# Optimization experiments

Measured on AMD Instinct MI355X. Metric: run time of the kernel, lower is better.

## Reference

```python
import jax, jax.numpy as jnp
import numpy as np

B, CIN, COUT, K, H, W = 8, 256, 256, 3, 128, 128


def setup_inputs() -> dict:
    key = jax.random.key(0)
    k1, k2, k3 = jax.random.split(key, 3)
    return {
        "input_vector": jax.random.normal(k1, (B, CIN, H, W), dtype=jnp.float32),
        "style_vector": jax.random.normal(k2, (B, CIN), dtype=jnp.float32),
        "weight": jax.random.normal(k3, (COUT, CIN, K, K), dtype=jnp.float32),
    }


def reference(input_vector, style_vector, weight):
    b, cin, h, w = input_vector.shape
    cout, _, k, _ = weight.shape
    # per-sample modulated weights: (b, O, I, k, k)
    ws = weight[None, :, :, :, :] * style_vector[:, None, :, None, None]
    # NOTE: faithful to source - sum over dims [1,2,3] = (O, I, kh), NOT kw.
    demod = jax.lax.rsqrt(jnp.sum(ws * ws, axis=(1, 2, 3), keepdims=True) + 1e-8)  # (b,1,1,1,k)
    ws = (ws * demod).reshape(b * cout, cin, k, k)
    x = input_vector.reshape(1, b * cin, h, w)
    # get_same_padding(W, k, dilation=1, stride=1) = (k-1)//2
    pad = ((w - 1) * (1 - 1) + 1 * (k - 1)) // 2
    out = jax.lax.conv_general_dilated(
        x, ws,
        window_strides=(1, 1),
        padding=[(pad, pad), (pad, pad)],
        feature_group_count=b,
        dimension_numbers=("NCHW", "OIHW", "NCHW"),
    )
    out = out.reshape(b, cout, h, w)
    return jax.nn.leaky_relu(out, negative_slope=0.2)
```

## Files before the change

kernel.cpp:

```cpp
#include <hip/hip_runtime.h>
#include <hip/hip_bf16.h>

#define B_    8
#define CIN   256
#define COUT  256
#define H_    128
#define W_    128
#define HP    130
#define WP    130

#define OCT   128
#define TROWS 8
#define TCOLS 32
#define XROWS 10
#define XCOLS 34
#define XCH   1360
#define XCHP  1536
#define CCS   ((size_t)COUT * CIN)

using bfrag = __attribute__((ext_vector_type(8))) short;
using f32x4 = __attribute__((ext_vector_type(4))) float;

#define ASM_VMCNT(n) asm volatile("s_waitcnt vmcnt(" #n ")" ::: "memory")
#define ASM_LGKM0()  asm volatile("s_waitcnt lgkmcnt(0)" ::: "memory")

__device__ __forceinline__ float leaky(float v) {
    return v >= 0.f ? v : 0.2f * v;
}

__device__ __forceinline__ unsigned short to_bf16(float v) {
    __hip_bfloat16 h = __float2bfloat16(v);
    return *(unsigned short*)&h;
}

__global__ void compute_S_kernel(const float* __restrict__ weight, float* __restrict__ S) {
    const int i = blockIdx.x;
    const int t = threadIdx.x;
    const float* wp = weight + ((size_t)t * CIN + i) * 9;
    float s0 = 0.f, s1 = 0.f, s2 = 0.f;
#pragma unroll
    for (int kh = 0; kh < 3; ++kh) {
        float a = wp[kh * 3 + 0], b = wp[kh * 3 + 1], c = wp[kh * 3 + 2];
        s0 = fmaf(a, a, s0); s1 = fmaf(b, b, s1); s2 = fmaf(c, c, s2);
    }
    __shared__ float red[3][256];
    red[0][t] = s0; red[1][t] = s1; red[2][t] = s2;
    __syncthreads();
    for (int off = 128; off > 0; off >>= 1) {
        if (t < off) {
            red[0][t] += red[0][t + off];
            red[1][t] += red[1][t + off];
            red[2][t] += red[2][t + off];
        }
        __syncthreads();
    }
    if (t == 0) {
        S[i * 3 + 0] = red[0][0];
        S[i * 3 + 1] = red[1][0];
        S[i * 3 + 2] = red[2][0];
    }
}

__global__ void compute_demod_kernel(const float* __restrict__ style,
                                     const float* __restrict__ S,
                                     float* __restrict__ demod) {
    const int b = blockIdx.x;
    const int t = threadIdx.x;
    float sv = style[b * CIN + t];
    float sv2 = sv * sv;
    float s0 = sv2 * S[t * 3 + 0];
    float s1 = sv2 * S[t * 3 + 1];
    float s2 = sv2 * S[t * 3 + 2];
    __shared__ float red[3][256];
    red[0][t] = s0; red[1][t] = s1; red[2][t] = s2;
    __syncthreads();
    for (int off = 128; off > 0; off >>= 1) {
        if (t < off) {
            red[0][t] += red[0][t + off];
            red[1][t] += red[1][t + off];
            red[2][t] += red[2][t + off];
        }
        __syncthreads();
    }
    if (t == 0) {
        demod[b * 3 + 0] = rsqrtf(red[0][0] + 1e-8f);
        demod[b * 3 + 1] = rsqrtf(red[1][0] + 1e-8f);
        demod[b * 3 + 2] = rsqrtf(red[2][0] + 1e-8f);
    }
}

__global__ void compute_wmodT_kernel(const float* __restrict__ weight,
                                     const float* __restrict__ style,
                                     const float* __restrict__ demod,
                                     unsigned short* __restrict__ wT) {
    const int bx = blockIdx.x;
    const int i  = threadIdx.x;
    const int o  = bx & (COUT - 1);
    const int j  = (bx >> 8) % 9;
    const int b  = bx / (9 * COUT);
    float w = weight[((size_t)o * CIN + i) * 9 + j];
    float m = style[b * CIN + i] * demod[b * 3 + (j % 3)];
    wT[(((size_t)(b * 9 + j) * COUT + o)) * CIN + i] = to_bf16(w * m);
}

__global__ __launch_bounds__(256) void transpose_kernel(const float* __restrict__ x,
                                                        unsigned short* __restrict__ xT) {
    const int bx = blockIdx.x;
    const int wtile = (bx & 3) * 32;
    const int itile = (bx >> 2) * 32;
    const int h = blockIdx.y;
    const int b = blockIdx.z;
    const int t = threadIdx.x;

    __shared__ float lt[32][33];

    {
        const int tw = t & 31, tr = t >> 5;
#pragma unroll
        for (int rr = 0; rr < 4; ++rr) {
            int il = tr + rr * 8;
            lt[il][tw] = x[(((size_t)b * CIN + itile + il) * H_ + h) * W_ + wtile + tw];
        }
    }
    __syncthreads();
    {
        const int il = t & 31, wr = t >> 5;
#pragma unroll
        for (int rr = 0; rr < 4; ++rr) {
            int wl = wr + rr * 8;
            xT[(((size_t)b * HP + (h + 1)) * WP + (wtile + wl + 1)) * CIN + itile + il] =
                to_bf16(lt[il][wl]);
        }
    }
}

__global__ void zero_border_kernel(unsigned short* __restrict__ xT) {
    const int b = blockIdx.x;
    const int r = blockIdx.y;
    const int t = threadIdx.x;
    int npix, base, stride;
    if (r == 0)      { npix = WP;  base = 0;                 stride = 1;  }
    else if (r == 1) { npix = WP;  base = (HP - 1) * WP;     stride = 1;  }
    else if (r == 2) { npix = 128; base = WP;                stride = WP; }
    else             { npix = 128; base = WP + (WP - 1);     stride = WP; }
    for (int idx = t; idx < npix * 32; idx += 256) {
        int p = idx >> 5, q = idx & 31;
        size_t off = ((size_t)b * HP * WP + base + (size_t)p * stride) * CIN;
        *(int4*)((unsigned short*)xT + off + q * 8) = (int4){0, 0, 0, 0};
    }
}

__global__ __launch_bounds__(256, 2) void conv_mfma_kernel(
    const unsigned short* __restrict__ xT,
    const unsigned short* __restrict__ wT,
    float* __restrict__ out)
{
    const int tid = threadIdx.x;
    const int lin = blockIdx.x;
    const int b    = lin & 7;
    const int rest = lin >> 3;
    const int oc0  = (rest & 1) * OCT;
    const int w0   = ((rest >> 1) & 3) * TCOLS;
    const int h0   = (rest >> 3) * TROWS;

    const int wid   = tid >> 6;
    const int lane  = tid & 63;
    const int wm    = wid >> 1;
    const int cw    = wid & 1;
    const int l15   = lane & 15;
    const int khalf = lane >> 4;

    __shared__ unsigned short lds_a[2][3 * OCT * 32];
    __shared__ unsigned short lds_x[XCHP * 8];

    const unsigned short* xb = xT + ((size_t)(b * HP + h0) * WP + w0) * CIN;
    const unsigned short* wb = wT + ((size_t)(b * 9) * COUT + oc0) * CIN;

    int offA[6];
#pragma unroll
    for (int j = 0; j < 6; ++j) {
        int c    = (wid * 6 + j) * 64 + lane;
        int slot = c & 3;
        int o    = (c >> 2) & 127;
        int kh   = c >> 9;
        offA[j] = (int)((size_t)(kh * 3) * CCS) + o * CIN
                  + ((slot ^ ((o >> 1) & 3)) << 3);
    }

    f32x4 acc[4][8];
#pragma unroll
    for (int m = 0; m < 4; ++m)
#pragma unroll
        for (int n = 0; n < 8; ++n) acc[m][n] = (f32x4){0.f, 0.f, 0.f, 0.f};

    auto stage_A = [&](unsigned short* dst, const unsigned short* wsrc) {
#pragma unroll
        for (int j = 0; j < 6; ++j) {
            __builtin_amdgcn_global_load_lds(
                (const __attribute__((address_space(1))) void*)(wsrc + offA[j]),
                (__attribute__((address_space(3))) void*)(dst + (wid * 6 + j) * 512),
                16, 0, 0);
        }
    };
    auto stage_X = [&](int i0) {
#pragma unroll
        for (int j = 0; j < 6; ++j) {
            int g  = (wid * 6 + j) * 64 + lane;
            int gg = g < XCH ? g : 0;
            int pix = gg >> 2, slot = gg & 3;
            int row = pix / XCOLS, col = pix - row * XCOLS;
            int ofx = (row * WP + col) * CIN + ((slot ^ ((col >> 1) & 3)) << 3);
            __builtin_amdgcn_global_load_lds(
                (const __attribute__((address_space(1))) void*)(xb + ofx + i0),
                (__attribute__((address_space(3))) void*)(lds_x + (wid * 6 + j) * 512),
                16, 0, 0);
        }
    };

    const int aoff = (wm * 64 + l15) * 32 + ((khalf ^ ((l15 >> 1) & 3)) << 3);

    auto compute = [&](int kw, const unsigned short* ab) {
        const int col = cw * 16 + l15 + kw;
        const unsigned short* bp = lds_x + col * 32 + ((khalf ^ ((col >> 1) & 3)) << 3);

        bfrag aF[3][4];
#pragma unroll
        for (int kh = 0; kh < 3; ++kh)
#pragma unroll
            for (int m = 0; m < 4; ++m)
                aF[kh][m] = *(const bfrag*)(ab + aoff + ((size_t)kh * 128 + m * 16) * 32);

        bfrag bs[3];
        bs[0] = *(const bfrag*)(bp);
        bs[1] = *(const bfrag*)(bp + (size_t)XCOLS * 32);

        __builtin_amdgcn_s_setprio(1);
#pragma unroll
        for (int r = 0; r < 10; ++r) {
            if (r < 8)
                bs[(r + 2) % 3] = *(const bfrag*)(bp + (size_t)(r + 2) * XCOLS * 32);
            const bfrag bv = bs[r % 3];
#pragma unroll
            for (int kh = 0; kh < 3; ++kh) {
                const int n = r - kh;
                if (n >= 0 && n < 8) {
#pragma unroll
                    for (int m = 0; m < 4; ++m)
                        acc[m][n] = __builtin_amdgcn_mfma_f32_16x16x32_bf16(
                            aF[kh][m], bv, acc[m][n], 0, 0, 0);
                }
            }
        }
        __builtin_amdgcn_s_setprio(0);
    };

    stage_X(0);
    stage_A(lds_a[0], wb);
    ASM_VMCNT(0);
    __builtin_amdgcn_s_barrier();
    __builtin_amdgcn_sched_barrier(0);

#define PHASE(KW, CUR, NXT, PRE_OFF)                                  \
    stage_A((NXT), wb + (PRE_OFF));                                   \
    ASM_VMCNT(6);                                                     \
    __builtin_amdgcn_s_barrier();                                     \
    __builtin_amdgcn_sched_barrier(0);                                \
    compute((KW), (CUR));                                             \
    ASM_LGKM0();                                                      \
    __builtin_amdgcn_s_barrier();                                     \
    __builtin_amdgcn_sched_barrier(0);

#pragma unroll 1
    for (int c = 0; c < 8; ++c) {
        unsigned short* pa = lds_a[c & 1];
        unsigned short* pb = lds_a[(c & 1) ^ 1];
        const size_t i0  = (size_t)c * 32;
        const size_t i0n = (size_t)((c + 1) & 7) * 32;

        PHASE(0, pa, pb, 1 * CCS + i0)
        PHASE(1, pb, pa, 2 * CCS + i0)
        PHASE(2, pa, pb, i0n)
        if (c < 7) stage_X((int)i0n);
    }
#undef PHASE
    ASM_VMCNT(0);

#pragma unroll
    for (int m = 0; m < 4; ++m) {
#pragma unroll
        for (int n = 0; n < 8; ++n) {
            int h = h0 + n;
            int w = w0 + cw * 16 + l15;
#pragma unroll
            for (int r = 0; r < 4; ++r) {
                int oc = oc0 + wm * 64 + m * 16 + khalf * 4 + r;
                out[(((size_t)b * COUT + oc) * H_ + h) * W_ + w] = leaky(acc[m][n][r]);
            }
        }
    }
}

extern "C" void kernel_launch(void* const* d_in, const int* in_sizes, int n_in,
                              void* d_out, int out_size, void* d_ws, size_t ws_size,
                              hipStream_t stream) {
    const float* x      = (const float*)d_in[0];
    const float* style  = (const float*)d_in[1];
    const float* weight = (const float*)d_in[2];
    float* out = (float*)d_out;

    float* S     = (float*)d_ws;
    float* demod = (float*)((char*)d_ws + 4096);
    unsigned short* wT = (unsigned short*)((char*)d_ws + 8192);
    unsigned short* xT = (unsigned short*)((char*)d_ws + 9445376);

    compute_S_kernel<<<CIN, 256, 0, stream>>>(weight, S);
    compute_demod_kernel<<<B_, 256, 0, stream>>>(style, S, demod);
    compute_wmodT_kernel<<<B_ * 9 * COUT, 256, 0, stream>>>(weight, style, demod, wT);
    transpose_kernel<<<dim3(32, H_, B_), 256, 0, stream>>>(x, xT);
    zero_border_kernel<<<dim3(B_, 4), 256, 0, stream>>>(xT);

    conv_mfma_kernel<<<dim3(1024), 256, 0, stream>>>(xT, wT, out);
}
```

Measured before the change: 182.2 us.

## Load weight fragments directly to registers and double-buffer input tile in LDS

Removes LDS staging of the modulated weights. Each wave now loads its A fragments straight from global memory into registers, prefetched during the tail of each kw sweep. The input tile becomes double-buffered in LDS so the next channel chunk streams in during the last sweep. This cuts per-phase barriers from six to one per chunk, at the cost of uncoalesced per-lane global loads for weights, more register pressure, and exposed global latency if the prefetch window is short.

New measurement: 218.4 us. 1.2x slower.

```diff
diff --git a/kernel.cpp b/kernel.cpp
--- a/kernel.cpp
+++ b/kernel.cpp
@@ -22,7 +22,6 @@
 using f32x4 = __attribute__((ext_vector_type(4))) float;
 
 #define ASM_VMCNT(n) asm volatile("s_waitcnt vmcnt(" #n ")" ::: "memory")
-#define ASM_LGKM0()  asm volatile("s_waitcnt lgkmcnt(0)" ::: "memory")
 
 __device__ __forceinline__ float leaky(float v) {
     return v >= 0.f ? v : 0.2f * v;
@@ -170,22 +169,11 @@
     const int l15   = lane & 15;
     const int khalf = lane >> 4;
 
-    __shared__ unsigned short lds_a[2][3 * OCT * 32];
-    __shared__ unsigned short lds_x[XCHP * 8];
+    __shared__ unsigned short lds_x[2][XCHP * 8];
 
     const unsigned short* xb = xT + ((size_t)(b * HP + h0) * WP + w0) * CIN;
-    const unsigned short* wb = wT + ((size_t)(b * 9) * COUT + oc0) * CIN;
-
-    int offA[6];
-#pragma unroll
-    for (int j = 0; j < 6; ++j) {
-        int c    = (wid * 6 + j) * 64 + lane;
-        int slot = c & 3;
-        int o    = (c >> 2) & 127;
-        int kh   = c >> 9;
-        offA[j] = (int)((size_t)(kh * 3) * CCS) + o * CIN
-                  + ((slot ^ ((o >> 1) & 3)) << 3);
-    }
+    const unsigned short* wbw = wT + ((size_t)(b * 9) * COUT + oc0 + wm * 64) * CIN;
+    const size_t alane = (size_t)l15 * CIN + khalf * 8;
 
     f32x4 acc[4][8];
 #pragma unroll
@@ -193,16 +181,9 @@
 #pragma unroll
         for (int n = 0; n < 8; ++n) acc[m][n] = (f32x4){0.f, 0.f, 0.f, 0.f};
 
-    auto stage_A = [&](unsigned short* dst, const unsigned short* wsrc) {
-#pragma unroll
-        for (int j = 0; j < 6; ++j) {
-            __builtin_amdgcn_global_load_lds(
-                (const __attribute__((address_space(1))) void*)(wsrc + offA[j]),
-                (__attribute__((address_space(3))) void*)(dst + (wid * 6 + j) * 512),
-                16, 0, 0);
-        }
-    };
-    auto stage_X = [&](int i0) {
+    bfrag aF[3][4];
+
+    auto stage_X = [&](int i0, unsigned short* dst) {
 #pragma unroll
         for (int j = 0; j < 6; ++j) {
             int g  = (wid * 6 + j) * 64 + lane;
@@ -212,29 +193,20 @@
             int ofx = (row * WP + col) * CIN + ((slot ^ ((col >> 1) & 3)) << 3);
             __builtin_amdgcn_global_load_lds(
                 (const __attribute__((address_space(1))) void*)(xb + ofx + i0),
-                (__attribute__((address_space(3))) void*)(lds_x + (wid * 6 + j) * 512),
+                (__attribute__((address_space(3))) void*)(dst + (wid * 6 + j) * 512),
                 16, 0, 0);
         }
     };
 
-    const int aoff = (wm * 64 + l15) * 32 + ((khalf ^ ((l15 >> 1) & 3)) << 3);
-
-    auto compute = [&](int kw, const unsigned short* ab) {
+    auto sweep = [&](int kw, const unsigned short* xcur, const unsigned short* an) {
         const int col = cw * 16 + l15 + kw;
-        const unsigned short* bp = lds_x + col * 32 + ((khalf ^ ((col >> 1) & 3)) << 3);
-
-        bfrag aF[3][4];
-#pragma unroll
-        for (int kh = 0; kh < 3; ++kh)
-#pragma unroll
-            for (int m = 0; m < 4; ++m)
-                aF[kh][m] = *(const bfrag*)(ab + aoff + ((size_t)kh * 128 + m * 16) * 32);
+        const unsigned short* bp =
+            xcur + col * 32 + ((khalf ^ ((col >> 1) & 3)) << 3);
 
         bfrag bs[3];
         bs[0] = *(const bfrag*)(bp);
         bs[1] = *(const bfrag*)(bp + (size_t)XCOLS * 32);
 
-        __builtin_amdgcn_s_setprio(1);
 #pragma unroll
         for (int r = 0; r < 10; ++r) {
             if (r < 8)
@@ -250,39 +222,41 @@
                             aF[kh][m], bv, acc[m][n], 0, 0, 0);
                 }
             }
-        }
-        __builtin_amdgcn_s_setprio(0);
+            if (r >= 7) {
+                const int kh = r - 7;
+#pragma unroll
+                for (int m = 0; m < 4; ++m)
+                    aF[kh][m] = *(const bfrag*)(an + (size_t)(kh * 3) * CCS
+                                                + (size_t)(m * 16) * CIN + alane);
+            }
+        }
     };
 
-    stage_X(0);
-    stage_A(lds_a[0], wb);
+    stage_X(0, lds_x[0]);
+#pragma unroll
+    for (int kh = 0; kh < 3; ++kh)
+#pragma unroll
+        for (int m = 0; m < 4; ++m)
+            aF[kh][m] = *(const bfrag*)(wbw + (size_t)(kh * 3) * CCS
+                                        + (size_t)(m * 16) * CIN + alane);
     ASM_VMCNT(0);
     __builtin_amdgcn_s_barrier();
     __builtin_amdgcn_sched_barrier(0);
 
-#define PHASE(KW, CUR, NXT, PRE_OFF)                                  \
-    stage_A((NXT), wb + (PRE_OFF));                                   \
-    ASM_VMCNT(6);                                                     \
-    __builtin_amdgcn_s_barrier();                                     \
-    __builtin_amdgcn_sched_barrier(0);                                \
-    compute((KW), (CUR));                                             \
-    ASM_LGKM0();                                                      \
-    __builtin_amdgcn_s_barrier();                                     \
-    __builtin_amdgcn_sched_barrier(0);
-
 #pragma unroll 1
     for (int c = 0; c < 8; ++c) {
-        unsigned short* pa = lds_a[c & 1];
-        unsigned short* pb = lds_a[(c & 1) ^ 1];
+        const unsigned short* xcur = lds_x[c & 1];
         const size_t i0  = (size_t)c * 32;
         const size_t i0n = (size_t)((c + 1) & 7) * 32;
 
-        PHASE(0, pa, pb, 1 * CCS + i0)
-        PHASE(1, pb, pa, 2 * CCS + i0)
-        PHASE(2, pa, pb, i0n)
-        if (c < 7) stage_X((int)i0n);
-    }
-#undef PHASE
+        sweep(0, xcur, wbw + 1 * CCS + i0);
+        sweep(1, xcur, wbw + 2 * CCS + i0);
+        if (c < 7) stage_X((int)i0n, lds_x[(c + 1) & 1]);
+        sweep(2, xcur, wbw + i0n);
+        ASM_VMCNT(12);
+        __builtin_amdgcn_s_barrier();
+        __builtin_amdgcn_sched_barrier(0);
+    }
     ASM_VMCNT(0);
 
 #pragma unroll
```

## Switch conv to 32x32x16 MFMA tiles and fold border zeroing into transpose

Applied to the files above, without the earlier changes.

Replaces the 16x16x32 bf16 MFMA tiling with 32x32x16 MFMAs: each wave now covers 32 output channels by 16 columns by two row groups, and the fragment addressing and epilogue mapping are reworked to match. The change aims for fewer A/B LDS fragment loads per FLOP and better MFMA throughput. The pipeline phases now add full vmcnt(0) waits, and the A prefetch for the second and third phases is issued after the barrier rather than before it, which may reduce overlap. Border zeroing moves into an extra slice of the transpose grid, removing one kernel launch.

Measured after the change: 202.5 us. +11.2%, slower.

```diff
diff --git a/kernel.cpp b/kernel.cpp
--- a/kernel.cpp
+++ b/kernel.cpp
@@ -18,8 +18,8 @@
 #define XCHP  1536
 #define CCS   ((size_t)COUT * CIN)
 
-using bfrag = __attribute__((ext_vector_type(8))) short;
-using f32x4 = __attribute__((ext_vector_type(4))) float;
+using bfrag  = __attribute__((ext_vector_type(8))) short;
+using f32x16 = __attribute__((ext_vector_type(16))) float;
 
 #define ASM_VMCNT(n) asm volatile("s_waitcnt vmcnt(" #n ")" ::: "memory")
 #define ASM_LGKM0()  asm volatile("s_waitcnt lgkmcnt(0)" ::: "memory")
@@ -106,14 +106,30 @@
 __global__ __launch_bounds__(256) void transpose_kernel(const float* __restrict__ x,
                                                         unsigned short* __restrict__ xT) {
     const int bx = blockIdx.x;
+    const int h  = blockIdx.y;
+    const int b  = blockIdx.z;
+    const int t  = threadIdx.x;
+    const int itile = (bx >> 2) * 32;
+
+    if (h == H_) {
+        const int q = bx & 3;
+        for (int idx = t; idx < 129 * 4; idx += 256) {
+            int px_i = idx >> 2, q4 = idx & 3;
+            int p = q * 129 + px_i;
+            int row, col;
+            if (p < 130)      { row = 0;       col = p; }
+            else if (p < 260) { row = HP - 1;  col = p - 130; }
+            else if (p < 388) { row = p - 259; col = 0; }
+            else              { row = p - 387; col = WP - 1; }
+            size_t off = ((size_t)b * HP * WP + (size_t)row * WP + col) * CIN
+                         + itile + q4 * 8;
+            *(int4*)((unsigned short*)xT + off) = (int4){0, 0, 0, 0};
+        }
+        return;
+    }
+
     const int wtile = (bx & 3) * 32;
-    const int itile = (bx >> 2) * 32;
-    const int h = blockIdx.y;
-    const int b = blockIdx.z;
-    const int t = threadIdx.x;
-
     __shared__ float lt[32][33];
-
     {
         const int tw = t & 31, tr = t >> 5;
 #pragma unroll
@@ -131,22 +147,6 @@
             xT[(((size_t)b * HP + (h + 1)) * WP + (wtile + wl + 1)) * CIN + itile + il] =
                 to_bf16(lt[il][wl]);
         }
-    }
-}
-
-__global__ void zero_border_kernel(unsigned short* __restrict__ xT) {
-    const int b = blockIdx.x;
-    const int r = blockIdx.y;
-    const int t = threadIdx.x;
-    int npix, base, stride;
-    if (r == 0)      { npix = WP;  base = 0;                 stride = 1;  }
-    else if (r == 1) { npix = WP;  base = (HP - 1) * WP;     stride = 1;  }
-    else if (r == 2) { npix = 128; base = WP;                stride = WP; }
-    else             { npix = 128; base = WP + (WP - 1);     stride = WP; }
-    for (int idx = t; idx < npix * 32; idx += 256) {
-        int p = idx >> 5, q = idx & 31;
-        size_t off = ((size_t)b * HP * WP + base + (size_t)p * stride) * CIN;
-        *(int4*)((unsigned short*)xT + off + q * 8) = (int4){0, 0, 0, 0};
     }
 }
 
@@ -163,12 +163,14 @@
     const int w0   = ((rest >> 1) & 3) * TCOLS;
     const int h0   = (rest >> 3) * TROWS;
 
-    const int wid   = tid >> 6;
-    const int lane  = tid & 63;
-    const int wm    = wid >> 1;
-    const int cw    = wid & 1;
-    const int l15   = lane & 15;
-    const int khalf = lane >> 4;
+    const int wid  = tid >> 6;
+    const int lane = tid & 63;
+    const int wm   = wid >> 1;
+    const int cw   = wid & 1;
+    const int l15  = lane & 15;
+    const int l31  = lane & 31;
+    const int ksl  = lane >> 5;
+    const int rowoff = ((lane >> 4) & 1) * 4;
 
     __shared__ unsigned short lds_a[2][3 * OCT * 32];
     __shared__ unsigned short lds_x[XCHP * 8];
@@ -187,11 +189,13 @@
                   + ((slot ^ ((o >> 1) & 3)) << 3);
     }
 
-    f32x4 acc[4][8];
-#pragma unroll
-    for (int m = 0; m < 4; ++m)
-#pragma unroll
-        for (int n = 0; n < 8; ++n) acc[m][n] = (f32x4){0.f, 0.f, 0.f, 0.f};
+    f32x16 acc[2][4];
+#pragma unroll
+    for (int m = 0; m < 2; ++m)
+#pragma unroll
+        for (int n = 0; n < 4; ++n)
+#pragma unroll
+            for (int e = 0; e < 16; ++e) acc[m][n][e] = 0.f;
 
     auto stage_A = [&](unsigned short* dst, const unsigned short* wsrc) {
 #pragma unroll
@@ -217,37 +221,49 @@
         }
     };
 
-    const int aoff = (wm * 64 + l15) * 32 + ((khalf ^ ((l15 >> 1) & 3)) << 3);
+    const int axor = (l31 >> 1) & 3;
+    const int abase = (wm * 64 + l31) * 32;
 
     auto compute = [&](int kw, const unsigned short* ab) {
-        const int col = cw * 16 + l15 + kw;
-        const unsigned short* bp = lds_x + col * 32 + ((khalf ^ ((col >> 1) & 3)) << 3);
-
-        bfrag aF[3][4];
+        const int col  = cw * 16 + l15 + kw;
+        const int bxor = (col >> 1) & 3;
+        const unsigned short* bp0 =
+            lds_x + ((rowoff) * XCOLS + col) * 32 + (((0 * 2 + ksl) ^ bxor) << 3);
+        const unsigned short* bp1 =
+            lds_x + ((rowoff) * XCOLS + col) * 32 + (((1 * 2 + ksl) ^ bxor) << 3);
+
+        bfrag aF[3][2][2];
 #pragma unroll
         for (int kh = 0; kh < 3; ++kh)
 #pragma unroll
-            for (int m = 0; m < 4; ++m)
-                aF[kh][m] = *(const bfrag*)(ab + aoff + ((size_t)kh * 128 + m * 16) * 32);
-
-        bfrag bs[3];
-        bs[0] = *(const bfrag*)(bp);
-        bs[1] = *(const bfrag*)(bp + (size_t)XCOLS * 32);
+            for (int m = 0; m < 2; ++m)
+#pragma unroll
+                for (int ks = 0; ks < 2; ++ks)
+                    aF[kh][m][ks] = *(const bfrag*)(ab + kh * (OCT * 32) + abase
+                                      + m * (32 * 32) + (((ks * 2 + ksl) ^ axor) << 3));
+
+        bfrag bs[2][2];
+        bs[0][0] = *(const bfrag*)(bp0);
+        bs[0][1] = *(const bfrag*)(bp1);
 
         __builtin_amdgcn_s_setprio(1);
 #pragma unroll
-        for (int r = 0; r < 10; ++r) {
-            if (r < 8)
-                bs[(r + 2) % 3] = *(const bfrag*)(bp + (size_t)(r + 2) * XCOLS * 32);
-            const bfrag bv = bs[r % 3];
+        for (int r = 0; r < 6; ++r) {
+            if (r < 5) {
+                bs[(r + 1) & 1][0] = *(const bfrag*)(bp0 + (size_t)(r + 1) * XCOLS * 32);
+                bs[(r + 1) & 1][1] = *(const bfrag*)(bp1 + (size_t)(r + 1) * XCOLS * 32);
+            }
 #pragma unroll
             for (int kh = 0; kh < 3; ++kh) {
-                const int n = r - kh;
-                if (n >= 0 && n < 8) {
-#pragma unroll
-                    for (int m = 0; m < 4; ++m)
-                        acc[m][n] = __builtin_amdgcn_mfma_f32_16x16x32_bf16(
-                            aF[kh][m], bv, acc[m][n], 0, 0, 0);
+                const int np = r - kh;
+                if (np >= 0 && np < 4) {
+#pragma unroll
+                    for (int m = 0; m < 2; ++m) {
+                        acc[m][np] = __builtin_amdgcn_mfma_f32_32x32x16_bf16(
+                            aF[kh][m][0], bs[r & 1][0], acc[m][np], 0, 0, 0);
+                        acc[m][np] = __builtin_amdgcn_mfma_f32_32x32x16_bf16(
+                            aF[kh][m][1], bs[r & 1][1], acc[m][np], 0, 0, 0);
+                    }
                 }
             }
         }
@@ -258,16 +274,6 @@
     stage_A(lds_a[0], wb);
     ASM_VMCNT(0);
     __builtin_amdgcn_s_barrier();
-    __builtin_amdgcn_sched_barrier(0);
-
-#define PHASE(KW, CUR, NXT, PRE_OFF)                                  \
-    stage_A((NXT), wb + (PRE_OFF));                                   \
-    ASM_VMCNT(6);                                                     \
-    __builtin_amdgcn_s_barrier();                                     \
-    __builtin_amdgcn_sched_barrier(0);                                \
-    compute((KW), (CUR));                                             \
-    ASM_LGKM0();                                                      \
-    __builtin_amdgcn_s_barrier();                                     \
     __builtin_amdgcn_sched_barrier(0);
 
 #pragma unroll 1
@@ -277,24 +283,38 @@
         const size_t i0  = (size_t)c * 32;
         const size_t i0n = (size_t)((c + 1) & 7) * 32;
 
-        PHASE(0, pa, pb, 1 * CCS + i0)
-        PHASE(1, pb, pa, 2 * CCS + i0)
-        PHASE(2, pa, pb, i0n)
+        stage_A(pb, wb + 1 * CCS + i0);
+        ASM_VMCNT(6);
+        __builtin_amdgcn_s_barrier();
+        __builtin_amdgcn_sched_barrier(0);
+        compute(0, pa);
+        ASM_LGKM0(); ASM_VMCNT(0);
+        __builtin_amdgcn_s_barrier();
+        __builtin_amdgcn_sched_barrier(0);
+        stage_A(pa, wb + 2 * CCS + i0);
+        compute(1, pb);
+        ASM_LGKM0(); ASM_VMCNT(0);
+        __builtin_amdgcn_s_barrier();
+        __builtin_amdgcn_sched_barrier(0);
+        stage_A(pb, wb + i0n);
+        compute(2, pa);
+        ASM_LGKM0(); ASM_VMCNT(0);
+        __builtin_amdgcn_s_barrier();
+        __builtin_amdgcn_sched_barrier(0);
         if (c < 7) stage_X((int)i0n);
     }
-#undef PHASE
     ASM_VMCNT(0);
 
 #pragma unroll
-    for (int m = 0; m < 4; ++m) {
-#pragma unroll
-        for (int n = 0; n < 8; ++n) {
-            int h = h0 + n;
+    for (int m = 0; m < 2; ++m) {
+#pragma unroll
+        for (int np = 0; np < 4; ++np) {
+            int h = h0 + np + rowoff;
             int w = w0 + cw * 16 + l15;
 #pragma unroll
-            for (int r = 0; r < 4; ++r) {
-                int oc = oc0 + wm * 64 + m * 16 + khalf * 4 + r;
-                out[(((size_t)b * COUT + oc) * H_ + h) * W_ + w] = leaky(acc[m][n][r]);
+            for (int r = 0; r < 16; ++r) {
+                int oc = oc0 + wm * 64 + m * 32 + ((r & 3) + 8 * (r >> 2) + 4 * ksl);
+                out[(((size_t)b * COUT + oc) * H_ + h) * W_ + w] = leaky(acc[m][np][r]);
             }
         }
     }
@@ -316,8 +336,7 @@
     compute_S_kernel<<<CIN, 256, 0, stream>>>(weight, S);
     compute_demod_kernel<<<B_, 256, 0, stream>>>(style, S, demod);
     compute_wmodT_kernel<<<B_ * 9 * COUT, 256, 0, stream>>>(weight, style, demod, wT);
-    transpose_kernel<<<dim3(32, H_, B_), 256, 0, stream>>>(x, xT);
-    zero_border_kernel<<<dim3(B_, 4), 256, 0, stream>>>(xT);
+    transpose_kernel<<<dim3(32, H_ + 1, B_), 256, 0, stream>>>(x, xT);
 
     conv_mfma_kernel<<<dim3(1024), 256, 0, stream>>>(xT, wT, out);
 }
```

## Prefetch next A fragments inside MFMA loop and fold border zeroing into transpose

Applied to the files above, without the earlier changes.

The conv kernel now loads the A-operand register fragments for the next kw phase during the tail of the current MFMA loop, so the LDS reads overlap with compute instead of sitting in front of it. The LDS buffer rotation and barrier schedule are rebuilt to fit this, with one barrier per phase and full vmcnt waits. The separate zero-border kernel is removed and its work moves into an extra row of transpose blocks, which saves one launch. In exchange the aF registers stay live across phases, raising register pressure, and the vmcnt(0) waits may expose global-load latency that the earlier partial waits hid.

Measured after the change: 185.5 us. Within noise of the previous version (+1.8%).

```diff
diff --git a/kernel.cpp b/kernel.cpp
--- a/kernel.cpp
+++ b/kernel.cpp
@@ -23,6 +23,7 @@
 
 #define ASM_VMCNT(n) asm volatile("s_waitcnt vmcnt(" #n ")" ::: "memory")
 #define ASM_LGKM0()  asm volatile("s_waitcnt lgkmcnt(0)" ::: "memory")
+#define BAR()  do { __builtin_amdgcn_s_barrier(); __builtin_amdgcn_sched_barrier(0); } while (0)
 
 __device__ __forceinline__ float leaky(float v) {
     return v >= 0.f ? v : 0.2f * v;
@@ -106,14 +107,30 @@
 __global__ __launch_bounds__(256) void transpose_kernel(const float* __restrict__ x,
                                                         unsigned short* __restrict__ xT) {
     const int bx = blockIdx.x;
+    const int h  = blockIdx.y;
+    const int b  = blockIdx.z;
+    const int t  = threadIdx.x;
+    const int itile = (bx >> 2) * 32;
+
+    if (h == H_) {
+        const int q = bx & 3;
+        for (int idx = t; idx < 129 * 4; idx += 256) {
+            int px_i = idx >> 2, q4 = idx & 3;
+            int p = q * 129 + px_i;
+            int row, col;
+            if (p < 130)      { row = 0;       col = p; }
+            else if (p < 260) { row = HP - 1;  col = p - 130; }
+            else if (p < 388) { row = p - 259; col = 0; }
+            else              { row = p - 387; col = WP - 1; }
+            size_t off = ((size_t)b * HP * WP + (size_t)row * WP + col) * CIN
+                         + itile + q4 * 8;
+            *(int4*)((unsigned short*)xT + off) = (int4){0, 0, 0, 0};
+        }
+        return;
+    }
+
     const int wtile = (bx & 3) * 32;
-    const int itile = (bx >> 2) * 32;
-    const int h = blockIdx.y;
-    const int b = blockIdx.z;
-    const int t = threadIdx.x;
-
     __shared__ float lt[32][33];
-
     {
         const int tw = t & 31, tr = t >> 5;
 #pragma unroll
@@ -131,22 +148,6 @@
             xT[(((size_t)b * HP + (h + 1)) * WP + (wtile + wl + 1)) * CIN + itile + il] =
                 to_bf16(lt[il][wl]);
         }
-    }
-}
-
-__global__ void zero_border_kernel(unsigned short* __restrict__ xT) {
-    const int b = blockIdx.x;
-    const int r = blockIdx.y;
-    const int t = threadIdx.x;
-    int npix, base, stride;
-    if (r == 0)      { npix = WP;  base = 0;                 stride = 1;  }
-    else if (r == 1) { npix = WP;  base = (HP - 1) * WP;     stride = 1;  }
-    else if (r == 2) { npix = 128; base = WP;                stride = WP; }
-    else             { npix = 128; base = WP + (WP - 1);     stride = WP; }
-    for (int idx = t; idx < npix * 32; idx += 256) {
-        int p = idx >> 5, q = idx & 31;
-        size_t off = ((size_t)b * HP * WP + base + (size_t)p * stride) * CIN;
-        *(int4*)((unsigned short*)xT + off + q * 8) = (int4){0, 0, 0, 0};
     }
 }
 
@@ -219,16 +220,19 @@
 
     const int aoff = (wm * 64 + l15) * 32 + ((khalf ^ ((l15 >> 1) & 3)) << 3);
 
-    auto compute = [&](int kw, const unsigned short* ab) {
+    bfrag aF[3][4];
+
+    auto loadA = [&](const unsigned short* ab) {
+#pragma unroll
+        for (int kh = 0; kh < 3; ++kh)
+#pragma unroll
+            for (int m = 0; m < 4; ++m)
+                aF[kh][m] = *(const bfrag*)(ab + aoff + ((size_t)kh * 128 + m * 16) * 32);
+    };
+
+    auto compute = [&](int kw, const unsigned short* abn) {
         const int col = cw * 16 + l15 + kw;
         const unsigned short* bp = lds_x + col * 32 + ((khalf ^ ((col >> 1) & 3)) << 3);
-
-        bfrag aF[3][4];
-#pragma unroll
-        for (int kh = 0; kh < 3; ++kh)
-#pragma unroll
-            for (int m = 0; m < 4; ++m)
-                aF[kh][m] = *(const bfrag*)(ab + aoff + ((size_t)kh * 128 + m * 16) * 32);
 
         bfrag bs[3];
         bs[0] = *(const bfrag*)(bp);
@@ -250,6 +254,13 @@
                             aF[kh][m], bv, acc[m][n], 0, 0, 0);
                 }
             }
+            if (r >= 7) {
+                const int kh = r - 7;
+#pragma unroll
+                for (int m = 0; m < 4; ++m)
+                    aF[kh][m] = *(const bfrag*)(abn + aoff
+                                  + ((size_t)kh * 128 + m * 16) * 32);
+            }
         }
         __builtin_amdgcn_s_setprio(0);
     };
@@ -257,32 +268,42 @@
     stage_X(0);
     stage_A(lds_a[0], wb);
     ASM_VMCNT(0);
-    __builtin_amdgcn_s_barrier();
-    __builtin_amdgcn_sched_barrier(0);
-
-#define PHASE(KW, CUR, NXT, PRE_OFF)                                  \
-    stage_A((NXT), wb + (PRE_OFF));                                   \
-    ASM_VMCNT(6);                                                     \
-    __builtin_amdgcn_s_barrier();                                     \
-    __builtin_amdgcn_sched_barrier(0);                                \
-    compute((KW), (CUR));                                             \
-    ASM_LGKM0();                                                      \
-    __builtin_amdgcn_s_barrier();                                     \
-    __builtin_amdgcn_sched_barrier(0);
+    BAR();
+    loadA(lds_a[0]);
+    ASM_LGKM0();
+    BAR();
+    stage_A(lds_a[1], wb + 1 * CCS);
+    ASM_VMCNT(0);
+    BAR();
 
 #pragma unroll 1
     for (int c = 0; c < 8; ++c) {
-        unsigned short* pa = lds_a[c & 1];
-        unsigned short* pb = lds_a[(c & 1) ^ 1];
+        unsigned short* be = lds_a[c & 1];
+        unsigned short* bo = lds_a[(c & 1) ^ 1];
         const size_t i0  = (size_t)c * 32;
         const size_t i0n = (size_t)((c + 1) & 7) * 32;
 
-        PHASE(0, pa, pb, 1 * CCS + i0)
-        PHASE(1, pb, pa, 2 * CCS + i0)
-        PHASE(2, pa, pb, i0n)
-        if (c < 7) stage_X((int)i0n);
-    }
-#undef PHASE
+        stage_A(be, wb + 2 * CCS + i0);
+        __builtin_amdgcn_sched_barrier(0);
+        compute(0, bo);
+        ASM_LGKM0(); ASM_VMCNT(0);
+        BAR();
+        stage_A(bo, wb + i0n);
+        __builtin_amdgcn_sched_barrier(0);
+        compute(1, be);
+        ASM_LGKM0(); ASM_VMCNT(0);
+        BAR();
+        stage_A(be, wb + 1 * CCS + i0n);
+        __builtin_amdgcn_sched_barrier(0);
+        compute(2, bo);
+        ASM_LGKM0(); ASM_VMCNT(0);
+        BAR();
+        if (c < 7) {
+            stage_X((int)i0n);
+            ASM_VMCNT(0);
+            BAR();
+        }
+    }
     ASM_VMCNT(0);
 
 #pragma unroll
@@ -316,8 +337,7 @@
     compute_S_kernel<<<CIN, 256, 0, stream>>>(weight, S);
     compute_demod_kernel<<<B_, 256, 0, stream>>>(style, S, demod);
     compute_wmodT_kernel<<<B_ * 9 * COUT, 256, 0, stream>>>(weight, style, demod, wT);
-    transpose_kernel<<<dim3(32, H_, B_), 256, 0, stream>>>(x, xT);
-    zero_border_kernel<<<dim3(B_, 4), 256, 0, stream>>>(xT);
+    transpose_kernel<<<dim3(32, H_ + 1, B_), 256, 0, stream>>>(x, xT);
 
     conv_mfma_kernel<<<dim3(1024), 256, 0, stream>>>(xT, wT, out);
 }
```
